# Kernel tuning notes

Measured on AMD Instinct MI355X. Metric: run time of the kernel, lower is better.

Reference implementation:

```python
import jax, jax.numpy as jnp
import numpy as np

# ---- static config (mirrors GridEncoder.__init__ kwargs) ----
INPUT_DIM = 3
NUM_LEVELS = 3          # CUDA wrapper hardcodes L = 3
LEVEL_DIM = 2           # C
PER_LEVEL_SCALE = 2.0
BASE_RESOLUTION = 128   # H
LOG2_HASHMAP_SIZE = 19
ALIGN_CORNERS = False
INTERP_ID = 0           # 0 = linear, 1 = smoothstep
B = 2097152             # number of query points
PLANE_H, PLANE_W = 1024, 512  # 3*PLANE_H*PLANE_W == offsets[-1]
PRIMES = (1, 2654435761, 805459861)  # instant-NGP spatial hash primes
S = float(np.log2(PER_LEVEL_SCALE))


def _compute_offsets():
    # replicates GridEncoder.__init__ offset construction
    offsets, offset = [], 0
    max_params = 2 ** LOG2_HASHMAP_SIZE
    for i in range(NUM_LEVELS):
        resolution = int(np.ceil(BASE_RESOLUTION * PER_LEVEL_SCALE ** i))
        params = min(max_params, (resolution if ALIGN_CORNERS else resolution + 1) ** INPUT_DIM)
        params = int(np.ceil(params / 8) * 8)
        offsets.append(offset)
        offset += params
    offsets.append(offset)
    return offsets


def setup_inputs() -> dict:
    key = jax.random.key(0)
    k1, k2 = jax.random.split(key)
    total = _compute_offsets()[-1]
    assert 3 * PLANE_H * PLANE_W == total, (total,)
    # learned triplane feature maps (embeddings.normal_(0, 0.1) in reset_parameters)
    triplane = 0.1 * jax.random.normal(k1, (3, LEVEL_DIM, PLANE_H, PLANE_W), dtype=jnp.float32)
    # query coordinates in [-bound, bound] = [-1, 1]
    inputs = jax.random.uniform(k2, (B, INPUT_DIM), dtype=jnp.float32, minval=-1.0, maxval=1.0)
    return {"triplane": triplane, "inputs": inputs}


def _grid_encode(x01, embeddings):
    # x01: [B, D] in [0,1]; embeddings: [offsets[-1], C] flat multi-level table
    offsets = _compute_offsets()
    D, C = INPUT_DIM, LEVEL_DIM
    n_corners = 2 ** D
    # binary corner offsets [8, 3]
    corners = jnp.array([[(i >> d) & 1 for d in range(D)] for i in range(n_corners)],
                        dtype=jnp.uint32)
    out = jnp.zeros((x01.shape[0], C), dtype=embeddings.dtype)
    for level in range(NUM_LEVELS):
        scale = 2.0 ** (level * S) * BASE_RESOLUTION - 1.0
        res = int(np.ceil(scale)) + 1
        hmap = offsets[level + 1] - offsets[level]
        pos = x01 * scale + (0.0 if ALIGN_CORNERS else 0.5)
        pos_grid = jnp.floor(pos)
        frac = pos - pos_grid                      # [B, D] in [0,1)
        if INTERP_ID == 1:  # smoothstep
            frac = frac * frac * (3.0 - 2.0 * frac)
        pg = pos_grid.astype(jnp.uint32)
        cp = pg[:, None, :] + corners[None, :, :]  # [B, 8, D] corner coords
        stride_dim = res if ALIGN_CORNERS else res + 1
        if stride_dim ** D > hmap:  # hash indexing (uint32 mult wraps, as in CUDA)
            p = jnp.array(PRIMES, dtype=jnp.uint32)
            h = cp * p
            idx = h[..., 0] ^ h[..., 1] ^ h[..., 2]
        else:  # dense (tiled) indexing
            strides = jnp.array([stride_dim ** d for d in range(D)], dtype=jnp.uint32)
            idx = jnp.sum(cp * strides, axis=-1, dtype=jnp.uint32)
        idx = (idx % jnp.uint32(hmap)).astype(jnp.int32) + offsets[level]  # [B, 8]
        feats = embeddings[idx]                    # [B, 8, C] gather
        # trilinear weights: prod over dims of frac / (1-frac) per corner bit
        w = jnp.prod(jnp.where(corners[None].astype(bool),
                               frac[:, None, :], 1.0 - frac[:, None, :]), axis=-1)  # [B, 8]
        out = out + jnp.einsum('bk,bkc->bc', w, feats)
    return out


def reference(triplane, inputs):
    bound = 1.0
    x01 = (inputs + bound) / (2.0 * bound)  # map to [0, 1]
    # triplane_.squeeze().permute(0,2,3,1).reshape(-1, level_dim)
    emb = jnp.transpose(triplane, (0, 2, 3, 1)).reshape(-1, LEVEL_DIM)
    return _grid_encode(x01, emb)  # [B, C]
```

## Files before the change

### kernel.cpp

```cpp
#include <hip/hip_runtime.h>
#include <hip/hip_fp16.h>


#define NPOINTS  2097152
#define HMASK    0x7FFFFu
#define PLANE    524288
#define NTAB     (3 * PLANE)

typedef float    floatx2 __attribute__((ext_vector_type(2)));
typedef unsigned uintx2  __attribute__((ext_vector_type(2)));
typedef unsigned uintx4  __attribute__((ext_vector_type(4)));

__device__ __forceinline__ unsigned pack2(float a, float b) {
    const __half2 h2 = __halves2half2(__float2half_rn(a), __float2half_rn(b));
    return *reinterpret_cast<const unsigned*>(&h2);
}

__global__ __launch_bounds__(256) void tp_convert_kernel(
    const float* __restrict__ tp, uintx4* __restrict__ tbl)
{
    const unsigned t = blockIdx.x * 256u + threadIdx.x;
    const unsigned level = t >> 17;
    const unsigned i4    = (t & 131071u) << 2;
    const float* __restrict__ b = tp + level * (2u * PLANE);
    const float4 c0 = *reinterpret_cast<const float4*>(b + i4);
    const float4 c1 = *reinterpret_cast<const float4*>(b + PLANE + i4);
    uintx4 o;
    o.x = pack2(c0.x, c1.x);
    o.y = pack2(c0.y, c1.y);
    o.z = pack2(c0.z, c1.z);
    o.w = pack2(c0.w, c1.w);
    tbl[t] = o;
}

__device__ __forceinline__ unsigned sel4(uintx4 q, unsigned o) {
    const unsigned a = (o & 1u) ? q.y : q.x;
    const unsigned b = (o & 1u) ? q.w : q.z;
    return (o & 2u) ? b : a;
}

__global__ __launch_bounds__(256) void grid_gather_kernel(
    const unsigned* __restrict__ tbl,
    const float* __restrict__ inputs,
    floatx2* __restrict__ out)
{
    const int i = blockIdx.x * 256 + threadIdx.x;

    const float x = __builtin_nontemporal_load(&inputs[3 * i + 0]);
    const float y = __builtin_nontemporal_load(&inputs[3 * i + 1]);
    const float z = __builtin_nontemporal_load(&inputs[3 * i + 2]);
    const float x0 = (x + 1.0f) * 0.5f;
    const float y0 = (y + 1.0f) * 0.5f;
    const float z0 = (z + 1.0f) * 0.5f;

    unsigned P0[12];
    unsigned dx[3];
    float rxs[3], rys[3], rzs[3];

#pragma unroll
    for (int level = 0; level < 3; ++level) {
        const float scale = (float)((128 << level) - 1);
        const float px = fmaf(x0, scale, 0.5f);
        const float py = fmaf(y0, scale, 0.5f);
        const float pz = fmaf(z0, scale, 0.5f);
        const float fx = floorf(px), fy = floorf(py), fz = floorf(pz);
        rxs[level] = px - fx; rys[level] = py - fy; rzs[level] = pz - fz;
        const unsigned gx = (unsigned)fx, gy = (unsigned)fy, gz = (unsigned)fz;

        dx[level] = gx ^ (gx + 1u);

        const unsigned hy0 = gy * 2654435761u;
        const unsigned hy1 = (gy + 1u) * 2654435761u;
        const unsigned hz0 = gz * 805459861u;
        const unsigned hz1 = (gz + 1u) * 805459861u;
        const unsigned lvl = (unsigned)level << 19;

        P0[level * 4 + 0] = lvl | ((gx ^ hy0 ^ hz0) & HMASK);
        P0[level * 4 + 1] = lvl | ((gx ^ hy1 ^ hz0) & HMASK);
        P0[level * 4 + 2] = lvl | ((gx ^ hy0 ^ hz1) & HMASK);
        P0[level * 4 + 3] = lvl | ((gx ^ hy1 ^ hz1) & HMASK);
    }

    unsigned e0[12], e1[12];

#pragma unroll
    for (int level = 0; level < 3; ++level) {
        const unsigned d = dx[level];
        if (d == 1u) {
#pragma unroll
            for (int j = 0; j < 4; ++j) {
                const unsigned P = P0[level * 4 + j];
                const uintx2 q = *reinterpret_cast<const uintx2*>(tbl + (P & ~1u));
                const unsigned o = P & 1u;
                e0[level * 4 + j] = o ? q.y : q.x;
                e1[level * 4 + j] = o ? q.x : q.y;
            }
        } else if (d == 3u) {
#pragma unroll
            for (int j = 0; j < 4; ++j) {
                const unsigned P = P0[level * 4 + j];
                const uintx4 q = *reinterpret_cast<const uintx4*>(tbl + (P & ~3u));
                const unsigned o = P & 3u;
                e0[level * 4 + j] = sel4(q, o);
                e1[level * 4 + j] = sel4(q, o ^ 3u);
            }
        } else {
#pragma unroll
            for (int j = 0; j < 4; ++j) {
                const unsigned P = P0[level * 4 + j];
                e0[level * 4 + j] = tbl[P];
                e1[level * 4 + j] = tbl[P ^ d];
            }
        }
    }

    float o0 = 0.0f, o1 = 0.0f;
#pragma unroll
    for (int level = 0; level < 3; ++level) {
        const float rx = rxs[level], ry = rys[level], rz = rzs[level];
        const float wx1 = rx, wx0 = 1.0f - rx;
        const float wy1 = ry, wy0 = 1.0f - ry;
        const float wz1 = rz, wz0 = 1.0f - rz;
        const float wyz[4] = { wy0 * wz0, wy1 * wz0, wy0 * wz1, wy1 * wz1 };
#pragma unroll
        for (int j = 0; j < 4; ++j) {
            const __half2 a = *reinterpret_cast<const __half2*>(&e0[level * 4 + j]);
            const __half2 b = *reinterpret_cast<const __half2*>(&e1[level * 4 + j]);
            const float2 fa = __half22float2(a);
            const float2 fb = __half22float2(b);
            const float wA = wx0 * wyz[j], wB = wx1 * wyz[j];
            o0 = fmaf(wA, fa.x, o0); o1 = fmaf(wA, fa.y, o1);
            o0 = fmaf(wB, fb.x, o0); o1 = fmaf(wB, fb.y, o1);
        }
    }

    floatx2 r; r.x = o0; r.y = o1;
    __builtin_nontemporal_store(r, &out[i]);
}

__global__ __launch_bounds__(256) void grid_fallback_kernel(
    const float* __restrict__ triplane,
    const float* __restrict__ inputs,
    float* __restrict__ out)
{
    const int i = blockIdx.x * blockDim.x + threadIdx.x;
    if (i >= NPOINTS) return;
    const float x0 = (inputs[3 * i + 0] + 1.0f) * 0.5f;
    const float y0 = (inputs[3 * i + 1] + 1.0f) * 0.5f;
    const float z0 = (inputs[3 * i + 2] + 1.0f) * 0.5f;
    float o0 = 0.0f, o1 = 0.0f;
#pragma unroll
    for (int level = 0; level < 3; ++level) {
        const float scale = (float)((128 << level) - 1);
        const float px = fmaf(x0, scale, 0.5f);
        const float py = fmaf(y0, scale, 0.5f);
        const float pz = fmaf(z0, scale, 0.5f);
        const float fx = floorf(px), fy = floorf(py), fz = floorf(pz);
        const float rx = px - fx, ry = py - fy, rz = pz - fz;
        const unsigned gx = (unsigned)fx, gy = (unsigned)fy, gz = (unsigned)fz;
        const float* __restrict__ base = triplane + level * (2 * PLANE);
#pragma unroll
        for (int c = 0; c < 8; ++c) {
            const unsigned bx = (c >> 0) & 1, by = (c >> 1) & 1, bz = (c >> 2) & 1;
            const unsigned h = (gx + bx) ^ ((gy + by) * 2654435761u) ^ ((gz + bz) * 805459861u);
            const unsigned local = h & HMASK;
            const float w = (bx ? rx : 1.0f - rx) * (by ? ry : 1.0f - ry) * (bz ? rz : 1.0f - rz);
            o0 = fmaf(w, base[local], o0);
            o1 = fmaf(w, base[PLANE + local], o1);
        }
    }
    reinterpret_cast<float2*>(out)[i] = make_float2(o0, o1);
}

extern "C" void kernel_launch(void* const* d_in, const int* in_sizes, int n_in,
                              void* d_out, int out_size, void* d_ws, size_t ws_size,
                              hipStream_t stream) {
    const float* triplane = (const float*)d_in[0];
    const float* inputs   = (const float*)d_in[1];
    const int threads = 256;
    const int gblocks = NPOINTS / threads;

    if (ws_size >= (size_t)NTAB * sizeof(unsigned)) {
        unsigned* tbl = (unsigned*)d_ws;
        tp_convert_kernel<<<(NTAB / 4) / threads, threads, 0, stream>>>(
            triplane, (uintx4*)tbl);
        grid_gather_kernel<<<gblocks, threads, 0, stream>>>(tbl, inputs, (floatx2*)d_out);
    } else {
        grid_fallback_kernel<<<gblocks, threads, 0, stream>>>(triplane, inputs, (float*)d_out);
    }
}
```

Measured before the change: 229.8 us.

## Process four points per thread level-by-level with block sync between levels

The gather kernel now launches a fixed grid of 2048 blocks, and each thread handles four points strided across the whole grid. Loop order changes to level-outer, point-inner, with a __syncthreads after each level. The intent looks like keeping every wave in a block on the same level's plane at the same time, for better L2 locality, while giving each thread more independent gathers in flight. The cost is more registers per thread and barrier stalls at each level.

```diff
diff --git a/kernel.cpp b/kernel.cpp
--- a/kernel.cpp
+++ b/kernel.cpp
@@ -6,6 +6,9 @@
 #define HMASK    0x7FFFFu
 #define PLANE    524288
 #define NTAB     (3 * PLANE)
+#define GBLOCKS  2048
+#define TTHREADS (GBLOCKS * 256)
+#define PPT      4
 
 typedef float    floatx2 __attribute__((ext_vector_type(2)));
 typedef unsigned uintx2  __attribute__((ext_vector_type(2)));
@@ -44,98 +47,101 @@
     const float* __restrict__ inputs,
     floatx2* __restrict__ out)
 {
-    const int i = blockIdx.x * 256 + threadIdx.x;
+    const int t = blockIdx.x * 256 + threadIdx.x;
 
-    const float x = __builtin_nontemporal_load(&inputs[3 * i + 0]);
-    const float y = __builtin_nontemporal_load(&inputs[3 * i + 1]);
-    const float z = __builtin_nontemporal_load(&inputs[3 * i + 2]);
-    const float x0 = (x + 1.0f) * 0.5f;
-    const float y0 = (y + 1.0f) * 0.5f;
-    const float z0 = (z + 1.0f) * 0.5f;
+    float x0[PPT], y0[PPT], z0[PPT];
+#pragma unroll
+    for (int p = 0; p < PPT; ++p) {
+        const int i = t + p * TTHREADS;
+        const float x = __builtin_nontemporal_load(&inputs[3 * i + 0]);
+        const float y = __builtin_nontemporal_load(&inputs[3 * i + 1]);
+        const float z = __builtin_nontemporal_load(&inputs[3 * i + 2]);
+        x0[p] = (x + 1.0f) * 0.5f;
+        y0[p] = (y + 1.0f) * 0.5f;
+        z0[p] = (z + 1.0f) * 0.5f;
+    }
 
-    unsigned P0[12];
-    unsigned dx[3];
-    float rxs[3], rys[3], rzs[3];
+    float o0[PPT], o1[PPT];
+#pragma unroll
+    for (int p = 0; p < PPT; ++p) { o0[p] = 0.0f; o1[p] = 0.0f; }
 
 #pragma unroll
     for (int level = 0; level < 3; ++level) {
         const float scale = (float)((128 << level) - 1);
-        const float px = fmaf(x0, scale, 0.5f);
-        const float py = fmaf(y0, scale, 0.5f);
-        const float pz = fmaf(z0, scale, 0.5f);
-        const float fx = floorf(px), fy = floorf(py), fz = floorf(pz);
-        rxs[level] = px - fx; rys[level] = py - fy; rzs[level] = pz - fz;
-        const unsigned gx = (unsigned)fx, gy = (unsigned)fy, gz = (unsigned)fz;
-
-        dx[level] = gx ^ (gx + 1u);
-
-        const unsigned hy0 = gy * 2654435761u;
-        const unsigned hy1 = (gy + 1u) * 2654435761u;
-        const unsigned hz0 = gz * 805459861u;
-        const unsigned hz1 = (gz + 1u) * 805459861u;
         const unsigned lvl = (unsigned)level << 19;
 
-        P0[level * 4 + 0] = lvl | ((gx ^ hy0 ^ hz0) & HMASK);
-        P0[level * 4 + 1] = lvl | ((gx ^ hy1 ^ hz0) & HMASK);
-        P0[level * 4 + 2] = lvl | ((gx ^ hy0 ^ hz1) & HMASK);
-        P0[level * 4 + 3] = lvl | ((gx ^ hy1 ^ hz1) & HMASK);
+#pragma unroll
+        for (int p = 0; p < PPT; ++p) {
+            const float px = fmaf(x0[p], scale, 0.5f);
+            const float py = fmaf(y0[p], scale, 0.5f);
+            const float pz = fmaf(z0[p], scale, 0.5f);
+            const float fx = floorf(px), fy = floorf(py), fz = floorf(pz);
+            const float rx = px - fx, ry = py - fy, rz = pz - fz;
+            const unsigned gx = (unsigned)fx, gy = (unsigned)fy, gz = (unsigned)fz;
+
+            const unsigned d = gx ^ (gx + 1u);
+            const unsigned hy0 = gy * 2654435761u;
+            const unsigned hy1 = (gy + 1u) * 2654435761u;
+            const unsigned hz0 = gz * 805459861u;
+            const unsigned hz1 = (gz + 1u) * 805459861u;
+
+            unsigned P0[4];
+            P0[0] = lvl | ((gx ^ hy0 ^ hz0) & HMASK);
+            P0[1] = lvl | ((gx ^ hy1 ^ hz0) & HMASK);
+            P0[2] = lvl | ((gx ^ hy0 ^ hz1) & HMASK);
+            P0[3] = lvl | ((gx ^ hy1 ^ hz1) & HMASK);
+
+            unsigned e0[4], e1[4];
+            if (d == 1u) {
+#pragma unroll
+                for (int j = 0; j < 4; ++j) {
+                    const unsigned P = P0[j];
+                    const uintx2 q = *reinterpret_cast<const uintx2*>(tbl + (P & ~1u));
+                    const unsigned o = P & 1u;
+                    e0[j] = o ? q.y : q.x;
+                    e1[j] = o ? q.x : q.y;
+                }
+            } else if (d == 3u) {
+#pragma unroll
+                for (int j = 0; j < 4; ++j) {
+                    const unsigned P = P0[j];
+                    const uintx4 q = *reinterpret_cast<const uintx4*>(tbl + (P & ~3u));
+                    const unsigned o = P & 3u;
+                    e0[j] = sel4(q, o);
+                    e1[j] = sel4(q, o ^ 3u);
+                }
+            } else {
+#pragma unroll
+                for (int j = 0; j < 4; ++j) {
+                    const unsigned P = P0[j];
+                    e0[j] = tbl[P];
+                    e1[j] = tbl[P ^ d];
+                }
+            }
+
+            const float wx1 = rx, wx0 = 1.0f - rx;
+            const float wy1 = ry, wy0 = 1.0f - ry;
+            const float wz1 = rz, wz0 = 1.0f - rz;
+            const float wyz[4] = { wy0 * wz0, wy1 * wz0, wy0 * wz1, wy1 * wz1 };
+#pragma unroll
+            for (int j = 0; j < 4; ++j) {
+                const __half2 a = *reinterpret_cast<const __half2*>(&e0[j]);
+                const __half2 b = *reinterpret_cast<const __half2*>(&e1[j]);
+                const float2 fa = __half22float2(a);
+                const float2 fb = __half22float2(b);
+                const float wA = wx0 * wyz[j], wB = wx1 * wyz[j];
+                o0[p] = fmaf(wA, fa.x, o0[p]); o1[p] = fmaf(wA, fa.y, o1[p]);
+                o0[p] = fmaf(wB, fb.x, o0[p]); o1[p] = fmaf(wB, fb.y, o1[p]);
+            }
+        }
+        __syncthreads();
     }
 
-    unsigned e0[12], e1[12];
-
 #pragma unroll
-    for (int level = 0; level < 3; ++level) {
-        const unsigned d = dx[level];
-        if (d == 1u) {
-#pragma unroll
-            for (int j = 0; j < 4; ++j) {
-                const unsigned P = P0[level * 4 + j];
-                const uintx2 q = *reinterpret_cast<const uintx2*>(tbl + (P & ~1u));
-                const unsigned o = P & 1u;
-                e0[level * 4 + j] = o ? q.y : q.x;
-                e1[level * 4 + j] = o ? q.x : q.y;
-            }
-        } else if (d == 3u) {
-#pragma unroll
-            for (int j = 0; j < 4; ++j) {
-                const unsigned P = P0[level * 4 + j];
-                const uintx4 q = *reinterpret_cast<const uintx4*>(tbl + (P & ~3u));
-                const unsigned o = P & 3u;
-                e0[level * 4 + j] = sel4(q, o);
-                e1[level * 4 + j] = sel4(q, o ^ 3u);
-            }
-        } else {
-#pragma unroll
-            for (int j = 0; j < 4; ++j) {
-                const unsigned P = P0[level * 4 + j];
-                e0[level * 4 + j] = tbl[P];
-                e1[level * 4 + j] = tbl[P ^ d];
-            }
-        }
+    for (int p = 0; p < PPT; ++p) {
+        floatx2 r; r.x = o0[p]; r.y = o1[p];
+        __builtin_nontemporal_store(r, &out[t + p * TTHREADS]);
     }
-
-    float o0 = 0.0f, o1 = 0.0f;
-#pragma unroll
-    for (int level = 0; level < 3; ++level) {
-        const float rx = rxs[level], ry = rys[level], rz = rzs[level];
-        const float wx1 = rx, wx0 = 1.0f - rx;
-        const float wy1 = ry, wy0 = 1.0f - ry;
-        const float wz1 = rz, wz0 = 1.0f - rz;
-        const float wyz[4] = { wy0 * wz0, wy1 * wz0, wy0 * wz1, wy1 * wz1 };
-#pragma unroll
-        for (int j = 0; j < 4; ++j) {
-            const __half2 a = *reinterpret_cast<const __half2*>(&e0[level * 4 + j]);
-            const __half2 b = *reinterpret_cast<const __half2*>(&e1[level * 4 + j]);
-            const float2 fa = __half22float2(a);
-            const float2 fb = __half22float2(b);
-            const float wA = wx0 * wyz[j], wB = wx1 * wyz[j];
-            o0 = fmaf(wA, fa.x, o0); o1 = fmaf(wA, fa.y, o1);
-            o0 = fmaf(wB, fb.x, o0); o1 = fmaf(wB, fb.y, o1);
-        }
-    }
-
-    floatx2 r; r.x = o0; r.y = o1;
-    __builtin_nontemporal_store(r, &out[i]);
 }
 
 __global__ __launch_bounds__(256) void grid_fallback_kernel(
@@ -178,14 +184,14 @@
     const float* triplane = (const float*)d_in[0];
     const float* inputs   = (const float*)d_in[1];
     const int threads = 256;
-    const int gblocks = NPOINTS / threads;
 
     if (ws_size >= (size_t)NTAB * sizeof(unsigned)) {
         unsigned* tbl = (unsigned*)d_ws;
         tp_convert_kernel<<<(NTAB / 4) / threads, threads, 0, stream>>>(
             triplane, (uintx4*)tbl);
-        grid_gather_kernel<<<gblocks, threads, 0, stream>>>(tbl, inputs, (floatx2*)d_out);
+        grid_gather_kernel<<<GBLOCKS, threads, 0, stream>>>(tbl, inputs, (floatx2*)d_out);
     } else {
-        grid_fallback_kernel<<<gblocks, threads, 0, stream>>>(triplane, inputs, (float*)d_out);
+        grid_fallback_kernel<<<NPOINTS / threads, threads, 0, stream>>>(
+            triplane, inputs, (float*)d_out);
     }
 }
```

New measurement: 198.4 us, median of 2. 1.16x faster.
